# Kernel tuning notes

Hardware: AMD Instinct MI355X
Metric: run time of the kernel (lower is better)

Reference implementation:

```python
import jax, jax.numpy as jnp
import numpy as np

# config constants inferred from source (GMVPD RPN head)
K_COMP = 5           # config.n_components (num_cell_anchors == 1, forced by gumbel_max reshape)
TEMP = 0.1           # config.gumbel_temperature
B, C = 2, 256
LEVELS = [(200, 336), (100, 168), (50, 84), (25, 42), (13, 21)]


def setup_inputs() -> dict:
    key = jax.random.key(0)
    ks = jax.random.split(key, 3 * len(LEVELS) + 3)
    inp = {}
    i = 0
    for l, (h, w) in enumerate(LEVELS):
        inp[f"feat{l}"] = jax.random.normal(ks[i], (B, C, h, w), jnp.float32); i += 1
        inp[f"eps{l}"] = jax.random.normal(ks[i], (B, 4 * K_COMP, h, w), jnp.float32); i += 1
        inp[f"gum{l}"] = jax.random.uniform(ks[i], (B, K_COMP, h, w), jnp.float32); i += 1
    # weights initialized with std=0.01, biases 0 (as in the torch init)
    inp["conv_w"] = 0.01 * jax.random.normal(ks[i], (C, C, 3, 3), jnp.float32); i += 1
    inp["conv_b"] = jnp.zeros((C,), jnp.float32)
    inp["cls_w"] = 0.01 * jax.random.normal(ks[i], (2, C), jnp.float32); i += 1
    inp["cls_b"] = jnp.zeros((2,), jnp.float32)
    inp["off_w"] = 0.01 * jax.random.normal(ks[i], (9 * K_COMP, C), jnp.float32); i += 1
    inp["off_b"] = jnp.zeros((9 * K_COMP,), jnp.float32)
    return inp


def _rpn_level(x, eps, u, conv_w, conv_b, cls_w, cls_b, off_w, off_b):
    # shared 3x3 conv + relu
    t = jax.lax.conv_general_dilated(x, conv_w, (1, 1), 'SAME',
                                     dimension_numbers=('NCHW', 'OIHW', 'NCHW'))
    t = jax.nn.relu(t + conv_b[None, :, None, None])
    # 1x1 heads as einsum
    cls = jnp.einsum('bchw,oc->bohw', t, cls_w) + cls_b[None, :, None, None]
    off = jnp.einsum('bchw,oc->bohw', t, off_w) + off_b[None, :, None, None]
    mean = off[:, :4 * K_COMP]
    lstd = off[:, 4 * K_COMP:8 * K_COMP]
    weight = off[:, 8 * K_COMP:]
    # gaussian reparameterization
    sample = mean + jnp.exp(lstd) * eps            # [B, 4K, H, W]
    # gumbel-softmax mixture weights over components
    g = -jnp.log(-jnp.log(u + 1e-10) + 1e-10)
    cw = jax.nn.softmax((g + weight) / TEMP, axis=1)  # [B, K, H, W]
    b, _, h, w = sample.shape
    # channel layout is k-major: channel = k*4 + j
    bbox = jnp.einsum('bkhw,bkjhw->bjhw', cw, sample.reshape(b, K_COMP, 4, h, w))
    return cls, bbox


def reference(feat0, eps0, gum0, feat1, eps1, gum1, feat2, eps2, gum2,
              feat3, eps3, gum3, feat4, eps4, gum4,
              conv_w, conv_b, cls_w, cls_b, off_w, off_b):
    feats = [feat0, feat1, feat2, feat3, feat4]
    epss = [eps0, eps1, eps2, eps3, eps4]
    gums = [gum0, gum1, gum2, gum3, gum4]
    outs = []
    for x, e, u in zip(feats, epss, gums):
        cls, bbox = _rpn_level(x, e, u, conv_w, conv_b, cls_w, cls_b, off_w, off_b)
        b = cls.shape[0]
        # pack per-level outputs: [B, H*W*2] cls + [B, H*W*4] bbox
        outs.append(jnp.concatenate([cls.transpose(0, 2, 3, 1).reshape(b, -1),
                                     bbox.transpose(0, 2, 3, 1).reshape(b, -1)], axis=1))
    return jnp.concatenate(outs, axis=1)  # [B, 537138]
```

## Files before the change

### kernel.cpp

```cpp
#include <hip/hip_runtime.h>


#define WT_F   (9*256*256)
#define PA_F   (3*8*64*8)
#define TOTAL_PER_B 537138L
#define NTILE  2799

typedef __attribute__((ext_vector_type(8))) _Float16 half8;
typedef __attribute__((ext_vector_type(4))) _Float16 half4;
typedef __attribute__((ext_vector_type(16))) float f32x16;
typedef __attribute__((ext_vector_type(4))) float f32x4;

struct ConvParams {
    const float* feat[5];
    long  toff[5];
    int   Hs[5], Ws[5], gxs[5], cum[5];
};
struct ProjParams {
    const float* eps[5];
    const float* gum[5];
    long  toff[5], loff[5], hws[5];
    int   tcum[5];
};

__global__ void prep_kernel(const float* __restrict__ conv_w,
                            const float* __restrict__ cls_w,
                            const float* __restrict__ off_w,
                            _Float16* __restrict__ wh,
                            _Float16* __restrict__ wl,
                            _Float16* __restrict__ pAh,
                            _Float16* __restrict__ pAl)
{
    int t = blockIdx.x * 256 + threadIdx.x;
    if (t < 8192) {
        int oc = t >> 5, cg = t & 31;
        const float4* s4 = (const float4*)(conv_w + ((long)oc * 256 + cg * 8) * 9);
        float w[72];
        #pragma unroll
        for (int i = 0; i < 18; i++) {
            float4 v = s4[i];
            w[i*4+0] = v.x; w[i*4+1] = v.y; w[i*4+2] = v.z; w[i*4+3] = v.w;
        }
        #pragma unroll
        for (int tap = 0; tap < 9; tap++) {
            half8 hv, lv;
            #pragma unroll
            for (int i = 0; i < 8; i++) {
                float x = w[i * 9 + tap];
                _Float16 h = (_Float16)x;
                hv[i] = h;
                lv[i] = (_Float16)(x - (float)h);
            }
            long o = ((long)(tap * 32 + cg) * 256 + oc) * 8;
            *(half8*)(wh + o) = hv;
            *(half8*)(wl + o) = lv;
        }
    }
    if (t < 1536) {
        int frag = t >> 6;
        int mt = frag >> 3, ks = frag & 7;
        int ln = t & 63;
        int m = mt * 16 + (ln & 15);
        int kb = ks * 32 + (ln >> 4) * 8;
        half8 hv, lv;
        #pragma unroll
        for (int i = 0; i < 8; i++) {
            int c = kb + i;
            float v = 0.f;
            if (m < 2)       v = cls_w[m * 256 + c];
            else if (m < 47) v = off_w[(m - 2) * 256 + c];
            _Float16 h = (_Float16)v;
            hv[i] = h;
            lv[i] = (_Float16)(v - (float)h);
        }
        *(half8*)(pAh + (long)t * 8) = hv;
        *(half8*)(pAl + (long)t * 8) = lv;
    }
}

__global__ __launch_bounds__(256, 2) void conv_all_kernel(
    ConvParams P,
    const _Float16* __restrict__ wh,
    const _Float16* __restrict__ wl,
    const float* __restrict__ bias,
    _Float16* __restrict__ tbuf)
{
    int tb = blockIdx.x;
    int l = 0;
    #pragma unroll
    for (int i = 0; i < 5; i++) if (tb >= P.cum[i]) l = i + 1;
    int prev = l ? P.cum[l - 1] : 0;
    int rem = tb - prev;
    const int gx = P.gxs[l];
    const int ty = rem / gx;
    const int tx = rem - ty * gx;
    const int H = P.Hs[l], W = P.Ws[l];
    const long hw = (long)H * W;
    const float* fb = P.feat[l] + (long)blockIdx.z * 256 * hw;
    _Float16* tl = tbuf + P.toff[l] + (long)blockIdx.z * hw * 256;

    __shared__ __align__(16) _Float16 sB[180 * 40];

    const int tid  = threadIdx.x;
    const int lane = tid & 63;
    const int wid  = tid >> 6;
    const int x0   = tx * 16;
    const int ty0  = ty * 8;
    const int oh   = wid >> 1;
    const int ph   = wid & 1;
    const int lr32 = lane & 31;
    const int kg   = lane >> 5;
    const int nrow = lr32 >> 4;
    const int ncol = lane & 15;

    f32x16 acc[4][2] = {};

    for (int c0 = 0; c0 < 256; c0 += 32) {
        __syncthreads();
        for (int e = tid; e < 720; e += 256) {
            int qg  = e / 180;
            int pos = e - qg * 180;
            int r   = pos / 18;
            int col = pos - r * 18;
            int gr = ty0 + r - 1;
            int gc = x0 + col - 1;
            half8 v = {};
            if (gr >= 0 && gr < H && gc >= 0 && gc < W) {
                const float* p = fb + (long)(c0 + qg * 8) * hw + (long)gr * W + gc;
                #pragma unroll
                for (int i = 0; i < 8; i++) { v[i] = (_Float16)(*p); p += hw; }
            }
            *(half8*)(sB + pos * 40 + qg * 8) = v;
        }
        __syncthreads();

        #pragma unroll
        for (int tap = 0; tap < 9; tap++) {
            const int dy = tap / 3;
            const int dx = tap - dy * 3;
            #pragma unroll
            for (int ks = 0; ks < 2; ks++) {
                const int cgt = (c0 >> 3) + ks * 2 + kg;
                const long ao = ((long)(tap * 32 + cgt) * 256 + oh * 128 + lr32) * 8;
                half8 Ah[4], Al[4];
                #pragma unroll
                for (int of = 0; of < 4; of++) {
                    Ah[of] = *(const half8*)(wh + ao + of * 256);
                    Al[of] = *(const half8*)(wl + ao + of * 256);
                }
                #pragma unroll
                for (int pf = 0; pf < 2; pf++) {
                    const int pos = (ph * 4 + pf * 2 + nrow + dy) * 18 + ncol + dx;
                    half8 Bv = *(const half8*)(sB + pos * 40 + ks * 16 + kg * 8);
                    #pragma unroll
                    for (int of = 0; of < 4; of++) {
                        acc[of][pf] = __builtin_amdgcn_mfma_f32_32x32x16_f16(Ah[of], Bv, acc[of][pf], 0, 0, 0);
                        acc[of][pf] = __builtin_amdgcn_mfma_f32_32x32x16_f16(Al[of], Bv, acc[of][pf], 0, 0, 0);
                    }
                }
            }
        }
    }

    const int x = x0 + ncol;
    if (x < W) {
        #pragma unroll
        for (int pf = 0; pf < 2; pf++) {
            const int row = ty0 + ph * 4 + pf * 2 + nrow;
            if (row < H) {
                long pb = ((long)row * W + x) * 256;
                #pragma unroll
                for (int of = 0; of < 4; of++) {
                    #pragma unroll
                    for (int q = 0; q < 4; q++) {
                        const int ob = oh * 128 + of * 32 + kg * 4 + 8 * q;
                        float4 b4 = *(const float4*)(bias + ob);
                        half4 hv;
                        hv[0] = (_Float16)fmaxf(acc[of][pf][q * 4 + 0] + b4.x, 0.f);
                        hv[1] = (_Float16)fmaxf(acc[of][pf][q * 4 + 1] + b4.y, 0.f);
                        hv[2] = (_Float16)fmaxf(acc[of][pf][q * 4 + 2] + b4.z, 0.f);
                        hv[3] = (_Float16)fmaxf(acc[of][pf][q * 4 + 3] + b4.w, 0.f);
                        *(half4*)(tl + pb + ob) = hv;
                    }
                }
            }
        }
    }
}

__global__ __launch_bounds__(256, 2) void proj_all_kernel(
    ProjParams P,
    const _Float16* __restrict__ tbuf,
    const _Float16* __restrict__ pAh,
    const _Float16* __restrict__ pAl,
    const float* __restrict__ cls_b,
    const float* __restrict__ off_b,
    float* __restrict__ out)
{
    __shared__ __align__(16) float sOut[4][64 * 52];
    const int tid  = threadIdx.x;
    const int lane = tid & 63;
    const int wid  = tid >> 6;

    int tile = blockIdx.x * 4 + wid;
    const bool tvalid = tile < NTILE;
    if (!tvalid) tile = NTILE - 1;
    int l = 0;
    #pragma unroll
    for (int i = 0; i < 5; i++) if (tile >= P.tcum[i]) l = i + 1;
    const int tprev = l ? P.tcum[l - 1] : 0;
    const long hw = P.hws[l];
    const long npx2 = 2 * hw;
    const long px0 = (long)(tile - tprev) * 64;
    const _Float16* tl = tbuf + P.toff[l];

    const int m16 = lane & 15;
    const int kq  = lane >> 4;

    f32x4 acc[3][4] = {};
    #pragma unroll
    for (int ks = 0; ks < 8; ks++) {
        half8 Ah[3], Al[3];
        #pragma unroll
        for (int mt = 0; mt < 3; mt++) {
            const long ao = (long)((mt * 8 + ks) * 64 + lane) * 8;
            Ah[mt] = *(const half8*)(pAh + ao);
            Al[mt] = *(const half8*)(pAl + ao);
        }
        #pragma unroll
        for (int nf = 0; nf < 4; nf++) {
            long px2 = px0 + nf * 16 + m16;
            if (px2 >= npx2) px2 = npx2 - 1;
            half8 Bv = *(const half8*)(tl + px2 * 256 + ks * 32 + kq * 8);
            #pragma unroll
            for (int mt = 0; mt < 3; mt++) {
                acc[mt][nf] = __builtin_amdgcn_mfma_f32_16x16x32_f16(Ah[mt], Bv, acc[mt][nf], 0, 0, 0);
                acc[mt][nf] = __builtin_amdgcn_mfma_f32_16x16x32_f16(Al[mt], Bv, acc[mt][nf], 0, 0, 0);
            }
        }
    }

    float* so = sOut[wid];
    #pragma unroll
    for (int nf = 0; nf < 4; nf++)
        #pragma unroll
        for (int mt = 0; mt < 3; mt++)
            *(f32x4*)(so + (nf * 16 + m16) * 52 + mt * 16 + kq * 4) = acc[mt][nf];
    __syncthreads();

    float v[48];
    #pragma unroll
    for (int j = 0; j < 12; j++) {
        f32x4 t4 = *(const f32x4*)(so + lane * 52 + j * 4);
        v[j*4+0] = t4[0]; v[j*4+1] = t4[1]; v[j*4+2] = t4[2]; v[j*4+3] = t4[3];
    }

    long px2 = px0 + lane;
    const bool pvalid = tvalid && (px2 < npx2);
    if (px2 >= npx2) px2 = npx2 - 1;
    const int b = px2 >= hw;
    const long pix = px2 - (b ? hw : 0);

    const float* eb = P.eps[l] + (long)b * 20 * hw + pix;
    const float* gb = P.gum[l] + (long)b * 5 * hw + pix;

    float wlog[5];
    float m = -1e30f;
    #pragma unroll
    for (int k = 0; k < 5; k++) {
        float u = gb[(long)k * hw];
        float g = -logf(-logf(u + 1e-10f) + 1e-10f);
        wlog[k] = (g + v[42 + k] + off_b[40 + k]) * 10.0f;
        m = fmaxf(m, wlog[k]);
    }
    float s = 0.f, cw[5];
    #pragma unroll
    for (int k = 0; k < 5; k++) { cw[k] = expf(wlog[k] - m); s += cw[k]; }
    float inv = 1.0f / s;

    float bbox[4] = {0.f, 0.f, 0.f, 0.f};
    #pragma unroll
    for (int k = 0; k < 5; k++) {
        float cwk = cw[k] * inv;
        #pragma unroll
        for (int j = 0; j < 4; j++) {
            int kj = k * 4 + j;
            float mean = v[2 + kj]  + off_b[kj];
            float lstd = v[22 + kj] + off_b[20 + kj];
            float sv = fmaf(expf(lstd), eb[(long)kj * hw], mean);
            bbox[j] = fmaf(cwk, sv, bbox[j]);
        }
    }

    if (pvalid) {
        float* ob = out + (long)b * TOTAL_PER_B + P.loff[l];
        float2 c2; c2.x = v[0] + cls_b[0]; c2.y = v[1] + cls_b[1];
        *(float2*)(ob + pix * 2) = c2;
        float* o2 = ob + hw * 2 + pix * 4;
        float2 b01; b01.x = bbox[0]; b01.y = bbox[1];
        float2 b23; b23.x = bbox[2]; b23.y = bbox[3];
        *(float2*)o2 = b01;
        *(float2*)(o2 + 2) = b23;
    }
}

extern "C" void kernel_launch(void* const* d_in, const int* in_sizes, int n_in,
                              void* d_out, int out_size, void* d_ws, size_t ws_size,
                              hipStream_t stream)
{
    static const int LH[5] = {200, 100, 50, 25, 13};
    static const int LW[5] = {336, 168, 84, 42, 21};

    const float* conv_w = (const float*)d_in[15];
    const float* conv_b = (const float*)d_in[16];
    const float* cls_w  = (const float*)d_in[17];
    const float* cls_b  = (const float*)d_in[18];
    const float* off_w  = (const float*)d_in[19];
    const float* off_b  = (const float*)d_in[20];

    _Float16* wh  = (_Float16*)d_ws;
    _Float16* wl  = wh + WT_F;
    _Float16* pAh = wl + WT_F;
    _Float16* pAl = pAh + PA_F;
    _Float16* tbuf = pAl + PA_F;

    ConvParams cp;
    ProjParams pp;
    long toff = 0, loff = 0;
    int cum = 0, tcum = 0;
    for (int l = 0; l < 5; l++) {
        int H = LH[l], W = LW[l];
        long hw = (long)H * W;
        cp.feat[l] = (const float*)d_in[3 * l];
        pp.eps[l]  = (const float*)d_in[3 * l + 1];
        pp.gum[l]  = (const float*)d_in[3 * l + 2];
        cp.toff[l] = toff; pp.toff[l] = toff;
        cp.Hs[l] = H; cp.Ws[l] = W;
        pp.hws[l] = hw;
        int gx = (W + 15) / 16, gy = (H + 7) / 8;
        cp.gxs[l] = gx;
        cum += gx * gy;
        cp.cum[l] = cum;
        pp.loff[l] = loff;
        tcum += (int)((2 * hw + 63) / 64);
        pp.tcum[l] = tcum;
        toff += 2L * hw * 256;
        loff += 6L * hw;
    }

    prep_kernel<<<32, 256, 0, stream>>>(conv_w, cls_w, off_w, wh, wl, pAh, pAl);

    conv_all_kernel<<<dim3((unsigned)cum, 1, 2), 256, 0, stream>>>(
        cp, wh, wl, conv_b, tbuf);

    proj_all_kernel<<<dim3((unsigned)((NTILE + 3) / 4)), 256, 0, stream>>>(
        pp, tbuf, pAh, pAl, cls_b, off_b, (float*)d_out);
}
```

Before: 699.9 us.

## Double-buffer conv input staging and retile to 32-wide pixels by 128 output channels

The 3x3 conv kernel now prefetches the next 32-channel input slice into registers while MFMAs run on the current LDS buffer, then writes it to a second LDS buffer. This removes one barrier per iteration and hides global-load latency behind compute. The tile changes from 16x8 pixels by 256 output channels to 32x8 pixels by 128 output channels, and the grid z dimension splits batch and output-channel half. Each input tile is therefore loaded twice, once per channel half. In exchange, LDS use doubles and the prefetch registers may raise register pressure.

Result: slower. 1.530 ms (+118.6%).

```diff
diff --git a/kernel.cpp b/kernel.cpp
--- a/kernel.cpp
+++ b/kernel.cpp
@@ -96,44 +96,76 @@
     const int tx = rem - ty * gx;
     const int H = P.Hs[l], W = P.Ws[l];
     const long hw = (long)H * W;
-    const float* fb = P.feat[l] + (long)blockIdx.z * 256 * hw;
-    _Float16* tl = tbuf + P.toff[l] + (long)blockIdx.z * hw * 256;
-
-    __shared__ __align__(16) _Float16 sB[180 * 40];
+    const int b   = blockIdx.z >> 1;
+    const int ocb = (blockIdx.z & 1) * 128;
+    const float* fb = P.feat[l] + (long)b * 256 * hw;
+    _Float16* tl = tbuf + P.toff[l] + (long)b * hw * 256;
+
+    __shared__ __align__(16) _Float16 sB[2][340 * 40];
 
     const int tid  = threadIdx.x;
     const int lane = tid & 63;
     const int wid  = tid >> 6;
-    const int x0   = tx * 16;
+    const int x0   = tx * 32;
     const int ty0  = ty * 8;
     const int oh   = wid >> 1;
     const int ph   = wid & 1;
     const int lr32 = lane & 31;
     const int kg   = lane >> 5;
-    const int nrow = lr32 >> 4;
-    const int ncol = lane & 15;
-
-    f32x16 acc[4][2] = {};
-
+
+    int s_qg[6], s_pos[6], s_gr[6], s_gc[6];
+    #pragma unroll
+    for (int i = 0; i < 6; i++) {
+        int e = i * 256 + tid;
+        if (e >= 1360) e = 1359;
+        int qg = e / 340;
+        int pos = e - qg * 340;
+        int r = pos / 34, col = pos - r * 34;
+        s_qg[i] = qg; s_pos[i] = pos;
+        s_gr[i] = ty0 + r - 1; s_gc[i] = x0 + col - 1;
+    }
+    const bool s_act5 = (5 * 256 + tid) < 1360;
+
+#define STAGE_LOAD(C0N, ST)                                                  \
+    {                                                                        \
+        _Pragma("unroll")                                                    \
+        for (int i = 0; i < 6; i++) {                                        \
+            half8 v = {};                                                    \
+            if ((i < 5 || s_act5) && s_gr[i] >= 0 && s_gr[i] < H &&          \
+                s_gc[i] >= 0 && s_gc[i] < W) {                               \
+                const float* p = fb + (long)((C0N) + s_qg[i] * 8) * hw +     \
+                                 (long)s_gr[i] * W + s_gc[i];                \
+                _Pragma("unroll")                                            \
+                for (int k = 0; k < 8; k++) { v[k] = (_Float16)(*p); p += hw; } \
+            }                                                                \
+            ST[i] = v;                                                       \
+        }                                                                    \
+    }
+
+#define STAGE_WRITE(DST, ST)                                                 \
+    {                                                                        \
+        _Pragma("unroll")                                                    \
+        for (int i = 0; i < 6; i++)                                          \
+            if (i < 5 || s_act5)                                             \
+                *(half8*)((DST) + s_pos[i] * 40 + s_qg[i] * 8) = ST[i];      \
+    }
+
+    f32x16 acc[2][4] = {};
+
+    {
+        half8 st0[6];
+        STAGE_LOAD(0, st0);
+        STAGE_WRITE(sB[0], st0);
+    }
+    __syncthreads();
+
+    #pragma unroll 1
     for (int c0 = 0; c0 < 256; c0 += 32) {
-        __syncthreads();
-        for (int e = tid; e < 720; e += 256) {
-            int qg  = e / 180;
-            int pos = e - qg * 180;
-            int r   = pos / 18;
-            int col = pos - r * 18;
-            int gr = ty0 + r - 1;
-            int gc = x0 + col - 1;
-            half8 v = {};
-            if (gr >= 0 && gr < H && gc >= 0 && gc < W) {
-                const float* p = fb + (long)(c0 + qg * 8) * hw + (long)gr * W + gc;
-                #pragma unroll
-                for (int i = 0; i < 8; i++) { v[i] = (_Float16)(*p); p += hw; }
-            }
-            *(half8*)(sB + pos * 40 + qg * 8) = v;
-        }
-        __syncthreads();
-
+        const int buf = (c0 >> 5) & 1;
+        half8 st[6];
+        if (c0 < 224) STAGE_LOAD(c0 + 32, st);
+
+        const _Float16* sb = sB[buf];
         #pragma unroll
         for (int tap = 0; tap < 9; tap++) {
             const int dy = tap / 3;
@@ -141,39 +173,49 @@
             #pragma unroll
             for (int ks = 0; ks < 2; ks++) {
                 const int cgt = (c0 >> 3) + ks * 2 + kg;
-                const long ao = ((long)(tap * 32 + cgt) * 256 + oh * 128 + lr32) * 8;
-                half8 Ah[4], Al[4];
-                #pragma unroll
-                for (int of = 0; of < 4; of++) {
-                    Ah[of] = *(const half8*)(wh + ao + of * 256);
-                    Al[of] = *(const half8*)(wl + ao + of * 256);
+                const long ao = ((long)(tap * 32 + cgt) * 256 + ocb + oh * 64 + lr32) * 8;
+                half8 Ah0 = *(const half8*)(wh + ao);
+                half8 Ah1 = *(const half8*)(wh + ao + 256);
+                half8 Al0 = *(const half8*)(wl + ao);
+                half8 Al1 = *(const half8*)(wl + ao + 256);
+
+                half8 Bv[4];
+                #pragma unroll
+                for (int pf = 0; pf < 4; pf++) {
+                    const int pos = (ph * 4 + pf + dy) * 34 + lr32 + dx;
+                    Bv[pf] = *(const half8*)(sb + pos * 40 + ks * 16 + kg * 8);
                 }
                 #pragma unroll
-                for (int pf = 0; pf < 2; pf++) {
-                    const int pos = (ph * 4 + pf * 2 + nrow + dy) * 18 + ncol + dx;
-                    half8 Bv = *(const half8*)(sB + pos * 40 + ks * 16 + kg * 8);
-                    #pragma unroll
-                    for (int of = 0; of < 4; of++) {
-                        acc[of][pf] = __builtin_amdgcn_mfma_f32_32x32x16_f16(Ah[of], Bv, acc[of][pf], 0, 0, 0);
-                        acc[of][pf] = __builtin_amdgcn_mfma_f32_32x32x16_f16(Al[of], Bv, acc[of][pf], 0, 0, 0);
-                    }
-                }
+                for (int pf = 0; pf < 4; pf++)
+                    acc[0][pf] = __builtin_amdgcn_mfma_f32_32x32x16_f16(Ah0, Bv[pf], acc[0][pf], 0, 0, 0);
+                #pragma unroll
+                for (int pf = 0; pf < 4; pf++)
+                    acc[1][pf] = __builtin_amdgcn_mfma_f32_32x32x16_f16(Ah1, Bv[pf], acc[1][pf], 0, 0, 0);
+                #pragma unroll
+                for (int pf = 0; pf < 4; pf++)
+                    acc[0][pf] = __builtin_amdgcn_mfma_f32_32x32x16_f16(Al0, Bv[pf], acc[0][pf], 0, 0, 0);
+                #pragma unroll
+                for (int pf = 0; pf < 4; pf++)
+                    acc[1][pf] = __builtin_amdgcn_mfma_f32_32x32x16_f16(Al1, Bv[pf], acc[1][pf], 0, 0, 0);
             }
         }
-    }
-
-    const int x = x0 + ncol;
+
+        if (c0 < 224) STAGE_WRITE(sB[buf ^ 1], st);
+        __syncthreads();
+    }
+
+    const int x = x0 + lr32;
     if (x < W) {
         #pragma unroll
-        for (int pf = 0; pf < 2; pf++) {
-            const int row = ty0 + ph * 4 + pf * 2 + nrow;
+        for (int pf = 0; pf < 4; pf++) {
+            const int row = ty0 + ph * 4 + pf;
             if (row < H) {
                 long pb = ((long)row * W + x) * 256;
                 #pragma unroll
-                for (int of = 0; of < 4; of++) {
+                for (int of = 0; of < 2; of++) {
                     #pragma unroll
                     for (int q = 0; q < 4; q++) {
-                        const int ob = oh * 128 + of * 32 + kg * 4 + 8 * q;
+                        const int ob = ocb + oh * 64 + of * 32 + kg * 4 + 8 * q;
                         float4 b4 = *(const float4*)(bias + ob);
                         half4 hv;
                         hv[0] = (_Float16)fmaxf(acc[of][pf][q * 4 + 0] + b4.x, 0.f);
@@ -186,6 +228,8 @@
             }
         }
     }
+#undef STAGE_LOAD
+#undef STAGE_WRITE
 }
 
 __global__ __launch_bounds__(256, 2) void proj_all_kernel(
@@ -337,7 +381,7 @@
         cp.toff[l] = toff; pp.toff[l] = toff;
         cp.Hs[l] = H; cp.Ws[l] = W;
         pp.hws[l] = hw;
-        int gx = (W + 15) / 16, gy = (H + 7) / 8;
+        int gx = (W + 31) / 32, gy = (H + 7) / 8;
         cp.gxs[l] = gx;
         cum += gx * gy;
         cp.cum[l] = cum;
@@ -350,7 +394,7 @@
 
     prep_kernel<<<32, 256, 0, stream>>>(conv_w, cls_w, off_w, wh, wl, pAh, pAl);
 
-    conv_all_kernel<<<dim3((unsigned)cum, 1, 2), 256, 0, stream>>>(
+    conv_all_kernel<<<dim3((unsigned)cum, 1, 4), 256, 0, stream>>>(
         cp, wh, wl, conv_b, tbuf);
 
     proj_all_kernel<<<dim3((unsigned)((NTILE + 3) / 4)), 256, 0, stream>>>(
```
